# Performance work log

Hardware: AMD Instinct MI355X
Metric: run time of the kernel (lower is better)

Reference implementation:

```python
import jax, jax.numpy as jnp
import numpy as np

B, DIM, H, W = 16, 512, 32, 32
N_CB, VOCAB, D_CB = 8, 1024, 64  # DIM == N_CB * D_CB


def setup_inputs() -> dict:
    key = jax.random.key(0)
    k1, k2 = jax.random.split(key)
    z = jax.random.normal(k1, (B, DIM, H, W), dtype=jnp.float32)
    codebooks = jax.random.normal(k2, (N_CB, VOCAB, D_CB), dtype=jnp.float32) * 0.02
    return {"z": z, "codebooks": codebooks}


def reference(z, codebooks):
    # Eval-mode forward of the multi-codebook (residual-style) VQ:
    # per-codebook squared-distance argmin, gather, straight-through, commitment loss.
    b, d, h, w = z.shape
    n_cb, vocab, d_cb = codebooks.shape
    # rearrange 'b d h w -> (b h w) d', then chunk d into n_cb contiguous parts
    z_flat = z.transpose(0, 2, 3, 1).reshape(-1, n_cb, d_cb)  # (N, n_cb, d_cb)
    # ||z||^2 - 2 z.c + ||c||^2  -> (N, n_cb, vocab)
    dists = (
        jnp.sum(z_flat * z_flat, axis=-1, keepdims=True)
        - 2.0 * jnp.einsum("ncd,cvd->ncv", z_flat, codebooks)
        + jnp.sum(codebooks * codebooks, axis=-1)[None, :, :]
    )
    idx = jnp.argmin(dists, axis=-1)  # (N, n_cb) int
    # gather per-codebook nearest embedding
    q = codebooks[jnp.arange(n_cb)[None, :], idx]  # (N, n_cb, d_cb)
    # commitment: mean over all elements (equal-size chunks => same as per-chunk mse averaged)
    commitment = jnp.mean((z_flat - jax.lax.stop_gradient(q)) ** 2)
    # straight-through estimator
    q_st = z_flat + jax.lax.stop_gradient(q - z_flat)
    quantized = q_st.reshape(b, h, w, d).transpose(0, 3, 1, 2)  # (B, D, H, W)
    indices = idx.reshape(b, h, w, n_cb).transpose(0, 3, 1, 2)  # (B, n_cb, H, W)
    return quantized, indices, commitment
```

## Files before the change

### kernel.cpp

```cpp
#include <hip/hip_runtime.h>
#include <float.h>

#define DIM   512
#define HW    1024
#define NCB   8
#define VOC   1024
#define DCB   64

#define THREADS   256
#define POS_TILE  128
#define VCHUNK    128
#define NCHUNK    8
#define CAP       16
#define MARGIN    0.012f

#define Q_ELEMS   8388608
#define I_ELEMS   131072
#define C_OFFSET  8519680

#define WS_CC_OFF 256
#define WS_CB_OFF 33024

typedef __attribute__((ext_vector_type(8))) short          short8;
typedef __attribute__((ext_vector_type(8))) unsigned short ushort8;
typedef __attribute__((ext_vector_type(4))) float          floatx4;

__device__ __forceinline__ unsigned short f2bf(float f) {
    unsigned u = __builtin_bit_cast(unsigned, f);
    unsigned r = u + 0x7FFFu + ((u >> 16) & 1u);
    return (unsigned short)(r >> 16);
}

__device__ __forceinline__ float np_sumsq64(const float v[64]) {
#pragma clang fp contract(off)
    float sq[64];
#pragma unroll
    for (int k = 0; k < 64; ++k) sq[k] = v[k] * v[k];
    float r[8];
#pragma unroll
    for (int j = 0; j < 8; ++j) r[j] = sq[j];
#pragma unroll
    for (int i = 8; i < 64; i += 8)
#pragma unroll
        for (int j = 0; j < 8; ++j) r[j] = r[j] + sq[i + j];
    return ((r[0] + r[1]) + (r[2] + r[3])) + ((r[4] + r[5]) + (r[6] + r[7]));
}

__device__ __forceinline__ float np_dist(const float zloc[64], const float c[64],
                                         float zz, float ccv) {
#pragma clang fp contract(off)
    float p[16];
#pragma unroll
    for (int l = 0; l < 16; ++l) p[l] = 0.f;
#pragma unroll
    for (int j = 0; j < 4; ++j)
#pragma unroll
        for (int l = 0; l < 16; ++l)
            p[l] = __builtin_fmaf(zloc[j * 16 + l], c[j * 16 + l], p[l]);
    float s8[8], s4[4];
#pragma unroll
    for (int l = 0; l < 8; ++l) s8[l] = p[l] + p[l + 8];
#pragma unroll
    for (int l = 0; l < 4; ++l) s4[l] = s8[l] + s8[l + 4];
    float u0 = s4[0] + s4[2];
    float u1 = s4[1] + s4[3];
    float E  = u0 + u1;
    float t  = zz - 2.0f * E;
    return t + ccv;
}

__global__ __launch_bounds__(256) void vq_prep_kernel(const float* __restrict__ cbk,
                                                      float* __restrict__ cc,
                                                      unsigned short* __restrict__ cbkBf) {
    int t = blockIdx.x * 256 + threadIdx.x;
    const float4* row = (const float4*)(cbk + (long)t * DCB);
    float c[64];
#pragma unroll
    for (int i = 0; i < 16; ++i) {
        float4 v = row[i];
        c[i * 4 + 0] = v.x; c[i * 4 + 1] = v.y;
        c[i * 4 + 2] = v.z; c[i * 4 + 3] = v.w;
    }
    cc[t] = np_sumsq64(c);
    const int swz = (t & 7) << 3;
#pragma unroll
    for (int g8 = 0; g8 < 8; ++g8) {
        ushort8 w;
#pragma unroll
        for (int e = 0; e < 8; ++e) w[e] = f2bf(-2.0f * c[g8 * 8 + e]);
        *(ushort8*)&cbkBf[(long)t * 64 + ((g8 * 8) ^ swz)] = w;
    }
}

struct SmemT {
    unsigned short zsb[POS_TILE * DCB];
    unsigned short csb[2][VCHUNK * DCB];
    float          ccS[VOC];
    unsigned       candI[POS_TILE * CAP];
    unsigned       cnt[POS_TILE];
    unsigned       idxF[POS_TILE];
    float          wred[4];
};

__device__ __forceinline__ void stage_cb(unsigned short* ldsDst,
                                         const unsigned short* gSrc,
                                         int wid, int lane) {
#pragma unroll
    for (int i = 0; i < 4; ++i) {
        const int off = wid * 2048 + i * 512;
        const unsigned short* g = gSrc + off + lane * 8;
        unsigned short* l = ldsDst + off;
        __builtin_amdgcn_global_load_lds(
            (const __attribute__((address_space(1))) unsigned int*)(const void*)g,
            (__attribute__((address_space(3))) unsigned int*)(void*)l,
            16, 0, 0);
    }
}

__global__ __launch_bounds__(THREADS, 2) void vq_main_kernel(
    const float* __restrict__ z, const float* __restrict__ cbk,
    const float* __restrict__ ccTab, const unsigned short* __restrict__ cbkBf,
    float* __restrict__ commitWs, unsigned* __restrict__ doneCnt,
    float* __restrict__ out)
{
    __shared__ SmemT sm;

    const int tid   = threadIdx.x;
    const int lane  = tid & 63;
    const int wid   = tid >> 6;
    const int l15   = lane & 15;
    const int lg    = lane >> 4;
    const int wpos0 = wid * 32;
    const int cb    = blockIdx.x & 7;
    const int tile  = blockIdx.x >> 3;
    const int b     = tile >> 3;
    const int hw0   = (tile & 7) * POS_TILE;

    const long zBase  = (long)b * (DIM * HW) + (long)cb * DCB * HW + hw0;
    const long cbBase = (long)cb * (VOC * DCB);
    const unsigned short* cbkBfCb = cbkBf + cbBase;

    stage_cb(sm.csb[0], cbkBfCb, wid, lane);

    for (int i = 0; i < 16; ++i) {
        int e   = i * THREADS + tid;
        int kp  = e >> 7;
        int pos = e & 127;
        int k   = kp * 2;
        float v0 = z[zBase + (long)k * HW + pos];
        float v1 = z[zBase + (long)(k + 1) * HW + pos];
        unsigned pack = (unsigned)f2bf(v0) | ((unsigned)f2bf(v1) << 16);
        *(unsigned*)&sm.zsb[pos * 64 + (k ^ ((pos & 7) << 3))] = pack;
    }
    ((float4*)sm.ccS)[tid] = ((const float4*)(ccTab + cb * VOC))[tid];
    if (tid < POS_TILE) sm.cnt[tid] = 0;
    __syncthreads();

    float runBest[2] = {FLT_MAX, FLT_MAX};
    int cur = 0;

    for (int chunk = 0; chunk < NCHUNK; ++chunk) {
        if (chunk < 7)
            stage_cb(sm.csb[cur ^ 1], cbkBfCb + (long)(chunk + 1) * VCHUNK * DCB, wid, lane);

        const unsigned short* cs = sm.csb[cur];

        floatx4 acc[8][2];
#pragma unroll
        for (int ct = 0; ct < 8; ++ct) {
            float4 ci = *(const float4*)&sm.ccS[chunk * VCHUNK + ct * 16 + lg * 4];
            floatx4 a = {ci.x, ci.y, ci.z, ci.w};
            acc[ct][0] = a; acc[ct][1] = a;
        }

#pragma unroll
        for (int ks = 0; ks < 2; ++ks) {
            short8 bz[2];
#pragma unroll
            for (int pt = 0; pt < 2; ++pt) {
                int row = wpos0 + pt * 16 + l15;
                bz[pt] = *(const short8*)&sm.zsb[row * 64 + ((ks * 32 + lg * 8) ^ ((row & 7) << 3))];
            }
#pragma unroll
            for (int ct = 0; ct < 8; ++ct) {
                int crow = ct * 16 + l15;
                short8 ac = *(const short8*)&cs[crow * 64 + ((ks * 32 + lg * 8) ^ ((crow & 7) << 3))];
#pragma unroll
                for (int pt = 0; pt < 2; ++pt)
                    acc[ct][pt] = __builtin_amdgcn_mfma_f32_16x16x32_bf16(ac, bz[pt], acc[ct][pt], 0, 0, 0);
            }
        }

#pragma unroll
        for (int pt = 0; pt < 2; ++pt) {
            float m = acc[0][pt][0];
#pragma unroll
            for (int ct = 0; ct < 8; ++ct)
#pragma unroll
                for (int r = 0; r < 4; ++r) m = fminf(m, acc[ct][pt][r]);
            m = fminf(m, __shfl_xor(m, 16, 64));
            m = fminf(m, __shfl_xor(m, 32, 64));
            runBest[pt] = fminf(runBest[pt], m);
            const float thr = runBest[pt] + MARGIN;
            const int pos = wpos0 + pt * 16 + l15;
#pragma unroll
            for (int ct = 0; ct < 8; ++ct)
#pragma unroll
                for (int r = 0; r < 4; ++r) {
                    if (acc[ct][pt][r] <= thr) {
                        unsigned idx  = chunk * VCHUNK + ct * 16 + lg * 4 + r;
                        unsigned slot = atomicAdd(&sm.cnt[pos], 1u);
                        if (slot < CAP) sm.candI[pos * CAP + slot] = idx;
                    }
                }
        }
        __syncthreads();
        cur ^= 1;
    }

    if (tid < POS_TILE) {
        const int pos = tid;
        float zloc[64];
#pragma unroll
        for (int k = 0; k < 64; ++k) zloc[k] = z[zBase + (long)k * HW + pos];
        const float zz = np_sumsq64(zloc);
        const unsigned n = sm.cnt[pos];
        float bd = FLT_MAX; unsigned bi = 0xFFFFFFFFu;
        if (n <= CAP) {
            for (unsigned s = 0; s < n; ++s) {
                unsigned vi = sm.candI[pos * CAP + s];
                const float4* cr = (const float4*)(cbk + cbBase + (long)vi * DCB);
                float c[64];
#pragma unroll
                for (int i = 0; i < 16; ++i) {
                    float4 v = cr[i];
                    c[i * 4 + 0] = v.x; c[i * 4 + 1] = v.y;
                    c[i * 4 + 2] = v.z; c[i * 4 + 3] = v.w;
                }
                float d = np_dist(zloc, c, zz, sm.ccS[vi]);
                if (d < bd || (d == bd && vi < bi)) { bd = d; bi = vi; }
            }
        } else {
            for (unsigned vi = 0; vi < VOC; ++vi) {
                const float4* cr = (const float4*)(cbk + cbBase + (long)vi * DCB);
                float c[64];
#pragma unroll
                for (int i = 0; i < 16; ++i) {
                    float4 v = cr[i];
                    c[i * 4 + 0] = v.x; c[i * 4 + 1] = v.y;
                    c[i * 4 + 2] = v.z; c[i * 4 + 3] = v.w;
                }
                float d = np_dist(zloc, c, zz, sm.ccS[vi]);
                if (d < bd) { bd = d; bi = vi; }
            }
        }
        sm.idxF[pos] = bi;
        out[Q_ELEMS + (long)b * (NCB * HW) + cb * HW + hw0 + pos] = (float)bi;
    }
    __syncthreads();

    {
        const int pos   = tid & 127;
        const int khalf = tid >> 7;
        const unsigned vi = sm.idxF[pos];
        const float* crow = cbk + cbBase + (long)vi * DCB + khalf * 32;
        const float* zp   = z + zBase + pos + (long)khalf * 32 * HW;
        float* qp = out + (long)b * (DIM * HW) + (long)(cb * DCB + khalf * 32) * HW + hw0 + pos;
        float csum = 0.f;
#pragma unroll
        for (int j4 = 0; j4 < 8; ++j4) {
            float4 cv = *(const float4*)(crow + j4 * 4);
            float z0 = zp[(long)(j4 * 4 + 0) * HW];
            float z1 = zp[(long)(j4 * 4 + 1) * HW];
            float z2 = zp[(long)(j4 * 4 + 2) * HW];
            float z3 = zp[(long)(j4 * 4 + 3) * HW];
            qp[(long)(j4 * 4 + 0) * HW] = (cv.x - z0) + z0;
            qp[(long)(j4 * 4 + 1) * HW] = (cv.y - z1) + z1;
            qp[(long)(j4 * 4 + 2) * HW] = (cv.z - z2) + z2;
            qp[(long)(j4 * 4 + 3) * HW] = (cv.w - z3) + z3;
            float d0 = z0 - cv.x; csum = fmaf(d0, d0, csum);
            float d1 = z1 - cv.y; csum = fmaf(d1, d1, csum);
            float d2 = z2 - cv.z; csum = fmaf(d2, d2, csum);
            float d3 = z3 - cv.w; csum = fmaf(d3, d3, csum);
        }
#pragma unroll
        for (int m = 1; m < 64; m <<= 1) csum += __shfl_xor(csum, m, 64);
        if (lane == 0) sm.wred[wid] = csum;
    }
    __syncthreads();

    if (tid == 0) {
        atomicAdd(commitWs, sm.wred[0] + sm.wred[1] + sm.wred[2] + sm.wred[3]);
        __threadfence();
        unsigned d = atomicAdd(doneCnt, 1u);
        if (d == 1023u) {
            __threadfence();
            float tot = atomicAdd(commitWs, 0.0f);
            out[C_OFFSET] = tot * (1.0f / 8388608.0f);
        }
    }
}

extern "C" void kernel_launch(void* const* d_in, const int* in_sizes, int n_in,
                              void* d_out, int out_size, void* d_ws, size_t ws_size,
                              hipStream_t stream) {
    (void)in_sizes; (void)n_in; (void)out_size; (void)ws_size;
    const float* z   = (const float*)d_in[0];
    const float* cbk = (const float*)d_in[1];
    float* out = (float*)d_out;
    char*  ws  = (char*)d_ws;
    float*          commitWs = (float*)ws;
    unsigned*       doneCnt  = (unsigned*)(ws + 4);
    float*          ccTab    = (float*)(ws + WS_CC_OFF);
    unsigned short* cbkBf    = (unsigned short*)(ws + WS_CB_OFF);

    hipMemsetAsync(d_ws, 0, 8, stream);
    vq_prep_kernel<<<dim3(32), dim3(256), 0, stream>>>(cbk, ccTab, cbkBf);
    vq_main_kernel<<<dim3(1024), dim3(THREADS), 0, stream>>>(z, cbk, ccTab, cbkBf,
                                                             commitWs, doneCnt, out);
}
```

Baseline: 196.8 us.

## Stage z tile in LDS for refinement and drop workspace memset

After the candidate-filter loop, the block loads its 64x128 fp32 z tile into LDS (reusing the codebook staging buffer) with coalesced float4 loads. The exact re-scoring and the quantize/commitment epilogue then read z from LDS instead of doing strided global loads, and the per-thread 64-register z copy is replaced by streamed LDS reads, which lowers register pressure. The workspace zeroing moves from a hipMemsetAsync into the prep kernel, and the prep kernel now runs as 64 blocks of 128 threads. The cost is an extra barrier and more LDS traffic during refinement.

```diff
diff --git a/kernel.cpp b/kernel.cpp
--- a/kernel.cpp
+++ b/kernel.cpp
@@ -31,48 +31,13 @@
     return (unsigned short)(r >> 16);
 }
 
-__device__ __forceinline__ float np_sumsq64(const float v[64]) {
-#pragma clang fp contract(off)
-    float sq[64];
-#pragma unroll
-    for (int k = 0; k < 64; ++k) sq[k] = v[k] * v[k];
-    float r[8];
-#pragma unroll
-    for (int j = 0; j < 8; ++j) r[j] = sq[j];
-#pragma unroll
-    for (int i = 8; i < 64; i += 8)
-#pragma unroll
-        for (int j = 0; j < 8; ++j) r[j] = r[j] + sq[i + j];
-    return ((r[0] + r[1]) + (r[2] + r[3])) + ((r[4] + r[5]) + (r[6] + r[7]));
-}
-
-__device__ __forceinline__ float np_dist(const float zloc[64], const float c[64],
-                                         float zz, float ccv) {
-#pragma clang fp contract(off)
-    float p[16];
-#pragma unroll
-    for (int l = 0; l < 16; ++l) p[l] = 0.f;
-#pragma unroll
-    for (int j = 0; j < 4; ++j)
-#pragma unroll
-        for (int l = 0; l < 16; ++l)
-            p[l] = __builtin_fmaf(zloc[j * 16 + l], c[j * 16 + l], p[l]);
-    float s8[8], s4[4];
-#pragma unroll
-    for (int l = 0; l < 8; ++l) s8[l] = p[l] + p[l + 8];
-#pragma unroll
-    for (int l = 0; l < 4; ++l) s4[l] = s8[l] + s8[l + 4];
-    float u0 = s4[0] + s4[2];
-    float u1 = s4[1] + s4[3];
-    float E  = u0 + u1;
-    float t  = zz - 2.0f * E;
-    return t + ccv;
-}
-
-__global__ __launch_bounds__(256) void vq_prep_kernel(const float* __restrict__ cbk,
+__global__ __launch_bounds__(128) void vq_prep_kernel(const float* __restrict__ cbk,
+                                                      char* __restrict__ ws,
                                                       float* __restrict__ cc,
                                                       unsigned short* __restrict__ cbkBf) {
-    int t = blockIdx.x * 256 + threadIdx.x;
+#pragma clang fp contract(off)
+    int t = blockIdx.x * 128 + threadIdx.x;
+    if (t == 0) { ((float*)ws)[0] = 0.f; ((unsigned*)ws)[1] = 0u; }
     const float4* row = (const float4*)(cbk + (long)t * DCB);
     float c[64];
 #pragma unroll
@@ -81,7 +46,14 @@
         c[i * 4 + 0] = v.x; c[i * 4 + 1] = v.y;
         c[i * 4 + 2] = v.z; c[i * 4 + 3] = v.w;
     }
-    cc[t] = np_sumsq64(c);
+    float r[8];
+#pragma unroll
+    for (int j = 0; j < 8; ++j) { float sq = c[j] * c[j]; r[j] = sq; }
+#pragma unroll
+    for (int i = 1; i < 8; ++i)
+#pragma unroll
+        for (int j = 0; j < 8; ++j) { float sq = c[i * 8 + j] * c[i * 8 + j]; r[j] = r[j] + sq; }
+    cc[t] = ((r[0] + r[1]) + (r[2] + r[3])) + ((r[4] + r[5]) + (r[6] + r[7]));
     const int swz = (t & 7) << 3;
 #pragma unroll
     for (int g8 = 0; g8 < 8; ++g8) {
@@ -115,6 +87,34 @@
             (__attribute__((address_space(3))) unsigned int*)(void*)l,
             16, 0, 0);
     }
+}
+
+__device__ __forceinline__ float np_dist_stream(const float* zcol, const float4* cr,
+                                                float zz, float ccv) {
+#pragma clang fp contract(off)
+    float p[16];
+#pragma unroll
+    for (int l = 0; l < 16; ++l) p[l] = 0.f;
+#pragma unroll
+    for (int j = 0; j < 4; ++j) {
+        float4 c0 = cr[j * 4 + 0], c1 = cr[j * 4 + 1];
+        float4 c2 = cr[j * 4 + 2], c3 = cr[j * 4 + 3];
+        float cl[16] = {c0.x, c0.y, c0.z, c0.w, c1.x, c1.y, c1.z, c1.w,
+                        c2.x, c2.y, c2.z, c2.w, c3.x, c3.y, c3.z, c3.w};
+#pragma unroll
+        for (int l = 0; l < 16; ++l)
+            p[l] = __builtin_fmaf(zcol[(long)(j * 16 + l) * POS_TILE], cl[l], p[l]);
+    }
+    float s8[8], s4[4];
+#pragma unroll
+    for (int l = 0; l < 8; ++l) s8[l] = p[l] + p[l + 8];
+#pragma unroll
+    for (int l = 0; l < 4; ++l) s4[l] = s8[l] + s8[l + 4];
+    float u0 = s4[0] + s4[2];
+    float u1 = s4[1] + s4[3];
+    float E  = u0 + u1;
+    float t  = zz - 2.0f * E;
+    return t + ccv;
 }
 
 __global__ __launch_bounds__(THREADS, 2) void vq_main_kernel(
@@ -218,39 +218,48 @@
         cur ^= 1;
     }
 
+    float* zf32 = (float*)sm.csb;
+#pragma unroll
+    for (int i = 0; i < 8; ++i) {
+        int e4   = i * THREADS + tid;
+        int k    = e4 >> 5;
+        int posq = e4 & 31;
+        float4 v = *(const float4*)(z + zBase + (long)k * HW + posq * 4);
+        *(float4*)&zf32[k * POS_TILE + posq * 4] = v;
+    }
+    __syncthreads();
+
     if (tid < POS_TILE) {
         const int pos = tid;
-        float zloc[64];
-#pragma unroll
-        for (int k = 0; k < 64; ++k) zloc[k] = z[zBase + (long)k * HW + pos];
-        const float zz = np_sumsq64(zloc);
+        const float* zcol = zf32 + pos;
+        float zz;
+        {
+#pragma clang fp contract(off)
+            float r[8];
+#pragma unroll
+            for (int j = 0; j < 8; ++j) { float v = zcol[(long)j * POS_TILE]; r[j] = v * v; }
+#pragma unroll
+            for (int i = 1; i < 8; ++i)
+#pragma unroll
+                for (int j = 0; j < 8; ++j) {
+                    float v = zcol[(long)(i * 8 + j) * POS_TILE];
+                    r[j] = r[j] + v * v;
+                }
+            zz = ((r[0] + r[1]) + (r[2] + r[3])) + ((r[4] + r[5]) + (r[6] + r[7]));
+        }
         const unsigned n = sm.cnt[pos];
         float bd = FLT_MAX; unsigned bi = 0xFFFFFFFFu;
         if (n <= CAP) {
             for (unsigned s = 0; s < n; ++s) {
                 unsigned vi = sm.candI[pos * CAP + s];
-                const float4* cr = (const float4*)(cbk + cbBase + (long)vi * DCB);
-                float c[64];
-#pragma unroll
-                for (int i = 0; i < 16; ++i) {
-                    float4 v = cr[i];
-                    c[i * 4 + 0] = v.x; c[i * 4 + 1] = v.y;
-                    c[i * 4 + 2] = v.z; c[i * 4 + 3] = v.w;
-                }
-                float d = np_dist(zloc, c, zz, sm.ccS[vi]);
+                float d = np_dist_stream(zcol, (const float4*)(cbk + cbBase + (long)vi * DCB),
+                                         zz, sm.ccS[vi]);
                 if (d < bd || (d == bd && vi < bi)) { bd = d; bi = vi; }
             }
         } else {
             for (unsigned vi = 0; vi < VOC; ++vi) {
-                const float4* cr = (const float4*)(cbk + cbBase + (long)vi * DCB);
-                float c[64];
-#pragma unroll
-                for (int i = 0; i < 16; ++i) {
-                    float4 v = cr[i];
-                    c[i * 4 + 0] = v.x; c[i * 4 + 1] = v.y;
-                    c[i * 4 + 2] = v.z; c[i * 4 + 3] = v.w;
-                }
-                float d = np_dist(zloc, c, zz, sm.ccS[vi]);
+                float d = np_dist_stream(zcol, (const float4*)(cbk + cbBase + (long)vi * DCB),
+                                         zz, sm.ccS[vi]);
                 if (d < bd) { bd = d; bi = vi; }
             }
         }
@@ -264,16 +273,16 @@
         const int khalf = tid >> 7;
         const unsigned vi = sm.idxF[pos];
         const float* crow = cbk + cbBase + (long)vi * DCB + khalf * 32;
-        const float* zp   = z + zBase + pos + (long)khalf * 32 * HW;
+        const float* zcol = zf32 + pos + khalf * 32 * POS_TILE;
         float* qp = out + (long)b * (DIM * HW) + (long)(cb * DCB + khalf * 32) * HW + hw0 + pos;
         float csum = 0.f;
 #pragma unroll
         for (int j4 = 0; j4 < 8; ++j4) {
             float4 cv = *(const float4*)(crow + j4 * 4);
-            float z0 = zp[(long)(j4 * 4 + 0) * HW];
-            float z1 = zp[(long)(j4 * 4 + 1) * HW];
-            float z2 = zp[(long)(j4 * 4 + 2) * HW];
-            float z3 = zp[(long)(j4 * 4 + 3) * HW];
+            float z0 = zcol[(j4 * 4 + 0) * POS_TILE];
+            float z1 = zcol[(j4 * 4 + 1) * POS_TILE];
+            float z2 = zcol[(j4 * 4 + 2) * POS_TILE];
+            float z3 = zcol[(j4 * 4 + 3) * POS_TILE];
             qp[(long)(j4 * 4 + 0) * HW] = (cv.x - z0) + z0;
             qp[(long)(j4 * 4 + 1) * HW] = (cv.y - z1) + z1;
             qp[(long)(j4 * 4 + 2) * HW] = (cv.z - z2) + z2;
@@ -314,8 +323,7 @@
     float*          ccTab    = (float*)(ws + WS_CC_OFF);
     unsigned short* cbkBf    = (unsigned short*)(ws + WS_CB_OFF);
 
-    hipMemsetAsync(d_ws, 0, 8, stream);
-    vq_prep_kernel<<<dim3(32), dim3(256), 0, stream>>>(cbk, ccTab, cbkBf);
+    vq_prep_kernel<<<dim3(64), dim3(128), 0, stream>>>(cbk, ws, ccTab, cbkBf);
     vq_main_kernel<<<dim3(1024), dim3(THREADS), 0, stream>>>(z, cbk, ccTab, cbkBf,
                                                              commitWs, doneCnt, out);
 }
```

New measurement: 193.4 us. About the same (-1.7%).
